# Kernel tuning notes

Hardware: AMD Instinct MI355X
Metric: run time of the kernel (lower is better)

The kernel has to match this reference:

```python
import jax, jax.numpy as jnp
import numpy as np

EMBED_DIM = 1024
NUM_HEADS = 16
HEAD_DIM = EMBED_DIM // NUM_HEADS
MAX_REL = 64
B, S = 4, 1024


def setup_inputs() -> dict:
    key = jax.random.key(0)
    ks = jax.random.split(key, 12)
    scale = 1.0 / np.sqrt(EMBED_DIM)
    inp = {
        "query": jax.random.normal(ks[0], (B, S, EMBED_DIM), jnp.float32),
        "key": jax.random.normal(ks[1], (B, S, EMBED_DIM), jnp.float32),
        "value": jax.random.normal(ks[2], (B, S, EMBED_DIM), jnp.float32),
        "attn_mask": jnp.ones((B, 1, S, S), jnp.int32),
        # projection weights stored [in, out] so x @ W matches torch Linear(x) with W = weight.T
        "Wq": jax.random.normal(ks[3], (EMBED_DIM, EMBED_DIM), jnp.float32) * scale,
        "bq": jnp.zeros((EMBED_DIM,), jnp.float32),
        "Wk": jax.random.normal(ks[4], (EMBED_DIM, EMBED_DIM), jnp.float32) * scale,
        "bk": jnp.zeros((EMBED_DIM,), jnp.float32),
        "Wv": jax.random.normal(ks[5], (EMBED_DIM, EMBED_DIM), jnp.float32) * scale,
        "bv": jnp.zeros((EMBED_DIM,), jnp.float32),
        "Wo": jax.random.normal(ks[6], (EMBED_DIM, EMBED_DIM), jnp.float32) * scale,
        "bo": jnp.zeros((EMBED_DIM,), jnp.float32),
        "rel_pos_embed": jax.random.normal(ks[7], (2 * MAX_REL + 1, HEAD_DIM), jnp.float32) * 0.02,
    }
    return inp


def _split_heads(x):
    # [B, S, E] -> [B, H, S, D]
    b, s, _ = x.shape
    return x.reshape(b, s, NUM_HEADS, HEAD_DIM).transpose(0, 2, 1, 3)


def reference(query, key, value, attn_mask, Wq, bq, Wk, bk, Wv, bv, Wo, bo, rel_pos_embed):
    q = _split_heads(query @ Wq + bq)
    k = _split_heads(key @ Wk + bk)
    v = _split_heads(value @ Wv + bv)

    scores = jnp.einsum("bhqd,bhkd->bhqk", q, k) / np.sqrt(HEAD_DIM).astype(np.float32)

    # relative position bias: rel_pos[i, j] = rel_pos_embed[clip(i - j) + MAX_REL]
    seq_len = scores.shape[-1]
    rng = jnp.arange(seq_len)
    range_mat = jnp.clip(rng[:, None] - rng[None, :], -MAX_REL, MAX_REL) + MAX_REL
    rel_pos = rel_pos_embed[range_mat]                       # [S, S, D]
    # torch: matmul(q[...,None,:], rel_pos.mT).squeeze(-2) == einsum over head_dim (NOT scaled)
    rel_scores = jnp.einsum("bhid,ijd->bhij", q, rel_pos)
    scores = scores + rel_scores

    scores = jnp.where(attn_mask == 0, -jnp.inf, scores)
    attn_weights = jax.nn.softmax(scores, axis=-1)           # dropout p=0.0 -> identity

    out = jnp.einsum("bhqk,bhkd->bhqd", attn_weights, v)
    out = out.transpose(0, 2, 1, 3).reshape(query.shape[0], -1, EMBED_DIM)
    out = out @ Wo + bo
    return out, attn_weights
```

## Files before the change

### kernel.cpp

```cpp
#include <hip/hip_runtime.h>
#include <math.h>

#define BB 4
#define SS 1024
#define EE 1024
#define HH 16
#define DD 64
#define RR 129
#define PRELW 130

typedef __attribute__((ext_vector_type(4))) float f32x4;
typedef __attribute__((ext_vector_type(8))) short bf8;
typedef __attribute__((ext_vector_type(4))) short s4v;

#define MFMA(a, b, c) __builtin_amdgcn_mfma_f32_16x16x32_bf16(a, b, c, 0, 0, 0)

__device__ __forceinline__ float bf2f(unsigned short u) {
    return __uint_as_float(((unsigned)u) << 16);
}
__device__ __forceinline__ unsigned short f2bf(float x) {
    unsigned u = __float_as_uint(x);
    return (unsigned short)((u + 0x7fffu + ((u >> 16) & 1u)) >> 16);
}

__global__ __launch_bounds__(256, 4)
void wtrans_kernel(const float* __restrict__ Wq, const float* __restrict__ Wk,
                   const float* __restrict__ Wv, const float* __restrict__ Wo,
                   unsigned short* __restrict__ wt_hi, unsigned short* __restrict__ wt_lo)
{
    __shared__ float T[64][65];
    const int w = blockIdx.z;
    const float* W = w == 0 ? Wq : (w == 1 ? Wk : (w == 2 ? Wv : Wo));
    const int n0 = blockIdx.x * 64, k0 = blockIdx.y * 64;
    const int tid = threadIdx.x;
#pragma unroll
    for (int i = 0; i < 4; ++i) {
        int c = tid + 256 * i; int r = c >> 4, c4 = c & 15;
        f32x4 v = *(const f32x4*)(W + (size_t)(k0 + r) * EE + n0 + c4 * 4);
        T[r][c4 * 4 + 0] = v.x; T[r][c4 * 4 + 1] = v.y;
        T[r][c4 * 4 + 2] = v.z; T[r][c4 * 4 + 3] = v.w;
    }
    __syncthreads();
#pragma unroll
    for (int i = 0; i < 4; ++i) {
        int c = tid + 256 * i; int r = c >> 4, c4 = c & 15;
        float x0 = T[c4 * 4 + 0][r], x1 = T[c4 * 4 + 1][r];
        float x2 = T[c4 * 4 + 2][r], x3 = T[c4 * 4 + 3][r];
        unsigned short h0 = f2bf(x0), h1 = f2bf(x1), h2 = f2bf(x2), h3 = f2bf(x3);
        unsigned short l0 = f2bf(x0 - bf2f(h0)), l1 = f2bf(x1 - bf2f(h1));
        unsigned short l2 = f2bf(x2 - bf2f(h2)), l3 = f2bf(x3 - bf2f(h3));
        size_t o = (size_t)w * 1048576 + (size_t)(n0 + r) * 1024 + k0 + c4 * 4;
        *(s4v*)&wt_hi[o] = (s4v){(short)h0, (short)h1, (short)h2, (short)h3};
        *(s4v*)&wt_lo[o] = (s4v){(short)l0, (short)l1, (short)l2, (short)l3};
    }
}

__global__ __launch_bounds__(256)
void maskbits_kernel(const int* __restrict__ mask, unsigned long long* __restrict__ mb)
{
    const int w = blockIdx.x * 256 + threadIdx.x;
    const int* p = mask + (size_t)w * 64;
    unsigned long long bits = 0;
#pragma unroll
    for (int i = 0; i < 16; ++i) {
        int4 v = *(const int4*)(p + i * 4);
        bits |= (unsigned long long)(v.x != 0) << (i * 4 + 0);
        bits |= (unsigned long long)(v.y != 0) << (i * 4 + 1);
        bits |= (unsigned long long)(v.z != 0) << (i * 4 + 2);
        bits |= (unsigned long long)(v.w != 0) << (i * 4 + 3);
    }
    mb[w] = bits;
}

template<int ASRC, int EPI>
__device__ __forceinline__ void gemm_body(
    const float* __restrict__ Af,
    const unsigned short* __restrict__ Ah_g, const unsigned short* __restrict__ Al_g,
    const unsigned short* __restrict__ Bh_g, const unsigned short* __restrict__ Bl_g,
    const float* __restrict__ bias,
    float* __restrict__ Yf, unsigned short* __restrict__ Yh, unsigned short* __restrict__ Yl,
    unsigned short* As_h, unsigned short* As_l, unsigned short* Bs_h, unsigned short* Bs_l,
    int m0, int n0)
{
    const int tid = threadIdx.x, lane = tid & 63, wid = tid >> 6;
    const int wm = (wid >> 1) * 64, wn = (wid & 1) * 64;
    f32x4 zero4 = {0.f, 0.f, 0.f, 0.f};
    f32x4 acc[4][4];
#pragma unroll
    for (int a = 0; a < 4; ++a)
#pragma unroll
        for (int b = 0; b < 4; ++b) acc[a][b] = zero4;

    for (int kt = 0; kt < 1024; kt += 64) {
        __syncthreads();
        if (ASRC == 0) {
#pragma unroll
            for (int i = 0; i < 8; ++i) {
                int c = tid + 256 * i; int r = c >> 4, c4 = c & 15;
                f32x4 v = *(const f32x4*)(Af + (size_t)(m0 + r) * 1024 + kt + c4 * 4);
                unsigned short h0 = f2bf(v.x), h1 = f2bf(v.y), h2 = f2bf(v.z), h3 = f2bf(v.w);
                unsigned short l0 = f2bf(v.x - bf2f(h0)), l1 = f2bf(v.y - bf2f(h1));
                unsigned short l2 = f2bf(v.z - bf2f(h2)), l3 = f2bf(v.w - bf2f(h3));
                int off = r * 64 + (((c4 >> 1) ^ (r & 7)) * 8) + (c4 & 1) * 4;
                *(s4v*)&As_h[off] = (s4v){(short)h0, (short)h1, (short)h2, (short)h3};
                *(s4v*)&As_l[off] = (s4v){(short)l0, (short)l1, (short)l2, (short)l3};
            }
        } else {
#pragma unroll
            for (int i = 0; i < 4; ++i) {
                int c = tid + 256 * i; int r = c >> 3, cc = c & 7;
                int off = r * 64 + ((cc ^ (r & 7)) * 8);
                *(bf8*)&As_h[off] = *(const bf8*)(Ah_g + (size_t)(m0 + r) * 1024 + kt + cc * 8);
                *(bf8*)&As_l[off] = *(const bf8*)(Al_g + (size_t)(m0 + r) * 1024 + kt + cc * 8);
            }
        }
#pragma unroll
        for (int i = 0; i < 4; ++i) {
            int c = tid + 256 * i; int r = c >> 3, cc = c & 7;
            int off = r * 64 + ((cc ^ (r & 7)) * 8);
            *(bf8*)&Bs_h[off] = *(const bf8*)(Bh_g + (size_t)(n0 + r) * 1024 + kt + cc * 8);
            *(bf8*)&Bs_l[off] = *(const bf8*)(Bl_g + (size_t)(n0 + r) * 1024 + kt + cc * 8);
        }
        __syncthreads();
#pragma unroll
        for (int ks = 0; ks < 2; ++ks) {
            bf8 ah[4], al[4], bh[4], bl[4];
#pragma unroll
            for (int f = 0; f < 4; ++f) {
                int ra = wm + f * 16 + (lane & 15);
                int ca = (ks * 4 + (lane >> 4)) ^ (ra & 7);
                ah[f] = *(const bf8*)&As_h[ra * 64 + ca * 8];
                al[f] = *(const bf8*)&As_l[ra * 64 + ca * 8];
                int rb = wn + f * 16 + (lane & 15);
                int cb = (ks * 4 + (lane >> 4)) ^ (rb & 7);
                bh[f] = *(const bf8*)&Bs_h[rb * 64 + cb * 8];
                bl[f] = *(const bf8*)&Bs_l[rb * 64 + cb * 8];
            }
#pragma unroll
            for (int fi = 0; fi < 4; ++fi)
#pragma unroll
                for (int fj = 0; fj < 4; ++fj) {
                    acc[fi][fj] = MFMA(ah[fi], bh[fj], acc[fi][fj]);
                    acc[fi][fj] = MFMA(al[fi], bh[fj], acc[fi][fj]);
                    acc[fi][fj] = MFMA(ah[fi], bl[fj], acc[fi][fj]);
                }
        }
    }
#pragma unroll
    for (int fi = 0; fi < 4; ++fi)
#pragma unroll
        for (int fj = 0; fj < 4; ++fj)
#pragma unroll
            for (int rg = 0; rg < 4; ++rg) {
                int m = m0 + wm + fi * 16 + ((lane >> 4) << 2) + rg;
                int n = n0 + wn + fj * 16 + (lane & 15);
                float val = acc[fi][fj][rg] + bias[n];
                if (EPI == 0) {
                    int b = m >> 10, s = m & 1023, h = n >> 6, d = n & 63;
                    size_t o = (((size_t)(b * 16 + h)) * 1024 + s) * 64 + d;
                    unsigned short hv = f2bf(val);
                    unsigned short lv = f2bf(val - bf2f(hv));
                    Yh[o] = hv; Yl[o] = lv;
                } else {
                    Yf[(size_t)m * 1024 + n] = val;
                }
            }
}

__global__ __launch_bounds__(256, 2)
void proj_qkv_kernel(const float* __restrict__ q_in, const float* __restrict__ k_in,
                     const float* __restrict__ v_in,
                     const unsigned short* __restrict__ wt_hi, const unsigned short* __restrict__ wt_lo,
                     const float* __restrict__ bq, const float* __restrict__ bk,
                     const float* __restrict__ bv,
                     unsigned short* qh_hi, unsigned short* qh_lo,
                     unsigned short* kh_hi, unsigned short* kh_lo,
                     unsigned short* vh_hi, unsigned short* vh_lo)
{
    __shared__ __align__(16) unsigned short As_h[128 * 64], As_l[128 * 64];
    __shared__ __align__(16) unsigned short Bs_h[128 * 64], Bs_l[128 * 64];
    const int z = blockIdx.z;
    const float* X = z == 0 ? q_in : (z == 1 ? k_in : v_in);
    const float* bias = z == 0 ? bq : (z == 1 ? bk : bv);
    unsigned short* Yh = z == 0 ? qh_hi : (z == 1 ? kh_hi : vh_hi);
    unsigned short* Yl = z == 0 ? qh_lo : (z == 1 ? kh_lo : vh_lo);
    gemm_body<0, 0>(X, nullptr, nullptr,
                    wt_hi + (size_t)z * 1048576, wt_lo + (size_t)z * 1048576,
                    bias, nullptr, Yh, Yl, As_h, As_l, Bs_h, Bs_l,
                    blockIdx.x * 128, blockIdx.y * 128);
}

__global__ __launch_bounds__(256, 2)
void outproj_kernel(const unsigned short* __restrict__ ctx_hi, const unsigned short* __restrict__ ctx_lo,
                    const unsigned short* __restrict__ wo_hi, const unsigned short* __restrict__ wo_lo,
                    const float* __restrict__ bo, float* __restrict__ out)
{
    __shared__ __align__(16) unsigned short As_h[128 * 64], As_l[128 * 64];
    __shared__ __align__(16) unsigned short Bs_h[128 * 64], Bs_l[128 * 64];
    gemm_body<1, 1>(nullptr, ctx_hi, ctx_lo, wo_hi, wo_lo, bo, out, nullptr, nullptr,
                    As_h, As_l, Bs_h, Bs_l, blockIdx.x * 128, blockIdx.y * 128);
}

__global__ __launch_bounds__(256, 4)
void vtrans_kernel(const unsigned short* __restrict__ vh_hi, const unsigned short* __restrict__ vh_lo,
                   unsigned short* __restrict__ vt_hi, unsigned short* __restrict__ vt_lo)
{
    __shared__ unsigned short T[64][72];
    const unsigned short* src = blockIdx.z ? vh_lo : vh_hi;
    unsigned short* dst = blockIdx.z ? vt_lo : vt_hi;
    const int st = blockIdx.x * 64, bh = blockIdx.y, tid = threadIdx.x;
#pragma unroll
    for (int i = 0; i < 4; ++i) {
        int c = tid + 256 * i; int r = c >> 4, d4 = c & 15;
        s4v v = *(const s4v*)(src + ((size_t)bh * 1024 + st + r) * 64 + d4 * 4);
        T[r][d4 * 4 + 0] = (unsigned short)v.x; T[r][d4 * 4 + 1] = (unsigned short)v.y;
        T[r][d4 * 4 + 2] = (unsigned short)v.z; T[r][d4 * 4 + 3] = (unsigned short)v.w;
    }
    __syncthreads();
#pragma unroll
    for (int i = 0; i < 4; ++i) {
        int c = tid + 256 * i; int r = c >> 4, s4_ = c & 15;
        s4v o = {(short)T[s4_ * 4 + 0][r], (short)T[s4_ * 4 + 1][r],
                 (short)T[s4_ * 4 + 2][r], (short)T[s4_ * 4 + 3][r]};
        *(s4v*)(dst + ((size_t)bh * 64 + r) * 1024 + st + s4_ * 4) = o;
    }
}

__global__ __launch_bounds__(256, 2)
void relproj_kernel(const unsigned short* __restrict__ qh_hi, const float* __restrict__ emb,
                    unsigned short* __restrict__ prel)
{
    __shared__ float se[RR][68];
    __shared__ float sq[128][68];
    const int tid = threadIdx.x;
    const size_t row0 = (size_t)blockIdx.x * 128;
    for (int i = tid; i < RR * 64; i += 256) { int r = i >> 6, d = i & 63; se[r][d] = emb[i]; }
#pragma unroll
    for (int i = 0; i < 8; ++i) {
        int c = tid + 256 * i; int r = c >> 4, d4 = c & 15;
        s4v v = *(const s4v*)(qh_hi + (row0 + r) * 64 + d4 * 4);
        sq[r][d4 * 4 + 0] = bf2f((unsigned short)v.x);
        sq[r][d4 * 4 + 1] = bf2f((unsigned short)v.y);
        sq[r][d4 * 4 + 2] = bf2f((unsigned short)v.z);
        sq[r][d4 * 4 + 3] = bf2f((unsigned short)v.w);
    }
    __syncthreads();
    for (int idx = tid; idx < 128 * RR; idx += 256) {
        int r = idx / RR, c = idx - r * RR;
        const float* a = sq[r];
        const float* b = se[c];
        float s = 0.f;
#pragma unroll
        for (int d = 0; d < 64; ++d) s = fmaf(a[d], b[d], s);
        prel[(row0 + r) * PRELW + c] = f2bf(s);
    }
}

__global__ __launch_bounds__(256, 2)
void scores_kernel(const unsigned short* __restrict__ qh_hi, const unsigned short* __restrict__ qh_lo,
                   const unsigned short* __restrict__ kh_hi, const unsigned short* __restrict__ kh_lo,
                   const unsigned short* __restrict__ prel, const unsigned long long* __restrict__ mb,
                   float* __restrict__ attn, float* __restrict__ rowm, float* __restrict__ rowsum)
{
    __shared__ __align__(16) unsigned short Sh[128 * 64], Sl[128 * 64];
    __shared__ __align__(16) unsigned short Pr[128 * PRELW];
    __shared__ float Sm[2][128], Ss[2][128];
    const int tid = threadIdx.x, lane = tid & 63, wid = tid >> 6;
    const int wi = wid >> 1, wj = wid & 1;
    const int g = lane >> 4, li = lane & 15;
    const int i0 = blockIdx.x * 128, bh = blockIdx.y, b = bh >> 4;

    const unsigned short* qbh = qh_hi + ((size_t)bh * 1024 + i0) * 64;
    const unsigned short* qbl = qh_lo + ((size_t)bh * 1024 + i0) * 64;
#pragma unroll
    for (int i = 0; i < 4; ++i) {
        int c = tid + 256 * i; int r = c >> 3, cc = c & 7;
        int off = r * 64 + ((cc ^ (r & 7)) * 8);
        *(bf8*)&Sh[off] = *(const bf8*)(qbh + r * 64 + cc * 8);
        *(bf8*)&Sl[off] = *(const bf8*)(qbl + r * 64 + cc * 8);
    }
    {
        const unsigned* src = (const unsigned*)(prel + ((size_t)bh * 1024 + i0) * PRELW);
        unsigned* dst = (unsigned*)Pr;
        for (int idx = tid; idx < 128 * (PRELW / 2); idx += 256) dst[idx] = src[idx];
    }
    __syncthreads();
    bf8 qfh[4][2], qfl[4][2];
#pragma unroll
    for (int fi = 0; fi < 4; ++fi)
#pragma unroll
        for (int ks = 0; ks < 2; ++ks) {
            int rb = wi * 64 + fi * 16 + li;
            int cb = (ks * 4 + g) ^ (rb & 7);
            qfh[fi][ks] = *(const bf8*)&Sh[rb * 64 + cb * 8];
            qfl[fi][ks] = *(const bf8*)&Sl[rb * 64 + cb * 8];
        }

    float rm[4], rs[4];
#pragma unroll
    for (int i = 0; i < 4; ++i) { rm[i] = -3.0e38f; rs[i] = 0.f; }

    for (int jt = 0; jt < 8; ++jt) {
        __syncthreads();
        const unsigned short* kbh = kh_hi + ((size_t)bh * 1024 + jt * 128) * 64;
        const unsigned short* kbl = kh_lo + ((size_t)bh * 1024 + jt * 128) * 64;
#pragma unroll
        for (int i = 0; i < 4; ++i) {
            int c = tid + 256 * i; int r = c >> 3, cc = c & 7;
            int off = r * 64 + ((cc ^ (r & 7)) * 8);
            *(bf8*)&Sh[off] = *(const bf8*)(kbh + r * 64 + cc * 8);
            *(bf8*)&Sl[off] = *(const bf8*)(kbl + r * 64 + cc * 8);
        }
        __syncthreads();
        f32x4 zero4 = {0.f, 0.f, 0.f, 0.f};
        f32x4 acc[4][4];
#pragma unroll
        for (int a = 0; a < 4; ++a)
#pragma unroll
            for (int c = 0; c < 4; ++c) acc[a][c] = zero4;
#pragma unroll
        for (int ks = 0; ks < 2; ++ks) {
            bf8 kfh[4], kfl[4];
#pragma unroll
            for (int fj = 0; fj < 4; ++fj) {
                int ra = wj * 64 + fj * 16 + li;
                int ca = (ks * 4 + g) ^ (ra & 7);
                kfh[fj] = *(const bf8*)&Sh[ra * 64 + ca * 8];
                kfl[fj] = *(const bf8*)&Sl[ra * 64 + ca * 8];
            }
#pragma unroll
            for (int fj = 0; fj < 4; ++fj)
#pragma unroll
                for (int fi = 0; fi < 4; ++fi) {
                    acc[fj][fi] = MFMA(kfh[fj], qfh[fi][ks], acc[fj][fi]);
                    acc[fj][fi] = MFMA(kfl[fj], qfh[fi][ks], acc[fj][fi]);
                    acc[fj][fi] = MFMA(kfh[fj], qfl[fi][ks], acc[fj][fi]);
                }
        }
#pragma unroll
        for (int fi = 0; fi < 4; ++fi) {
            const int rowL = wi * 64 + fi * 16 + li;
            const int ii = i0 + rowL;
            const unsigned long long mw = mb[((size_t)b * 1024 + ii) * 16 + jt * 2 + wj];
            float p16[4][4];
            float tmax = -3.0e38f;
#pragma unroll
            for (int fj = 0; fj < 4; ++fj)
#pragma unroll
                for (int rg = 0; rg < 4; ++rg) {
                    int jloc = fj * 16 + g * 4 + rg;
                    int jj = jt * 128 + wj * 64 + jloc;
                    int dd = ii - jj; dd = dd < -64 ? -64 : (dd > 64 ? 64 : dd);
                    float s = acc[fj][fi][rg] * 0.125f + bf2f(Pr[rowL * PRELW + dd + 64]);
                    if (!((mw >> jloc) & 1ull)) s = -1.0e30f;
                    p16[fj][rg] = s;
                    tmax = fmaxf(tmax, s);
                }
            tmax = fmaxf(tmax, __shfl_xor(tmax, 16, 64));
            tmax = fmaxf(tmax, __shfl_xor(tmax, 32, 64));
            float nm = fmaxf(rm[fi], tmax);
            float ps = 0.f;
#pragma unroll
            for (int fj = 0; fj < 4; ++fj)
#pragma unroll
                for (int rg = 0; rg < 4; ++rg) ps += __expf(p16[fj][rg] - nm);
            ps += __shfl_xor(ps, 16, 64);
            ps += __shfl_xor(ps, 32, 64);
            rs[fi] = rs[fi] * __expf(rm[fi] - nm) + ps;
            rm[fi] = nm;
            float* arow = attn + ((size_t)bh * 1024 + ii) * 1024 + jt * 128 + wj * 64 + g * 4;
#pragma unroll
            for (int fj = 0; fj < 4; ++fj) {
                f32x4 st = {p16[fj][0], p16[fj][1], p16[fj][2], p16[fj][3]};
                *(f32x4*)(arow + fj * 16) = st;
            }
        }
    }
#pragma unroll
    for (int fi = 0; fi < 4; ++fi) {
        if (lane < 16) {
            Sm[wj][wi * 64 + fi * 16 + li] = rm[fi];
            Ss[wj][wi * 64 + fi * 16 + li] = rs[fi];
        }
    }
    __syncthreads();
    if (tid < 128) {
        float m0_ = Sm[0][tid], m1_ = Sm[1][tid];
        float mm = fmaxf(m0_, m1_);
        float ss = Ss[0][tid] * __expf(m0_ - mm) + Ss[1][tid] * __expf(m1_ - mm);
        rowm[(size_t)bh * 1024 + i0 + tid] = mm;
        rowsum[(size_t)bh * 1024 + i0 + tid] = ss;
    }
}

__global__ __launch_bounds__(256, 2)
void pv_kernel(float* __restrict__ attn,
               const unsigned short* __restrict__ vt_hi, const unsigned short* __restrict__ vt_lo,
               const float* __restrict__ rowm, const float* __restrict__ rowsum,
               unsigned short* __restrict__ ctx_hi, unsigned short* __restrict__ ctx_lo)
{
    __shared__ __align__(16) unsigned short Ah[128 * 64], Al[128 * 64];
    __shared__ __align__(16) unsigned short Bh_[64 * 64], Bl_[64 * 64];
    const int tid = threadIdx.x, lane = tid & 63, wid = tid >> 6;
    const int i0 = blockIdx.x * 128, bh = blockIdx.y;

    float m8[8], inv8[8];
#pragma unroll
    for (int i = 0; i < 8; ++i) {
        int r = (tid >> 4) + 16 * i;
        m8[i] = rowm[(size_t)bh * 1024 + i0 + r];
        inv8[i] = 1.f / rowsum[(size_t)bh * 1024 + i0 + r];
    }
    f32x4 zero4 = {0.f, 0.f, 0.f, 0.f};
    f32x4 acc[2][4];
#pragma unroll
    for (int a = 0; a < 2; ++a)
#pragma unroll
        for (int c = 0; c < 4; ++c) acc[a][c] = zero4;

    for (int jt = 0; jt < 16; ++jt) {
        __syncthreads();
#pragma unroll
        for (int i = 0; i < 8; ++i) {
            int c = tid + 256 * i; int r = c >> 4, c4 = c & 15;
            size_t gidx = ((size_t)bh * 1024 + i0 + r) * 1024 + jt * 64 + c4 * 4;
            f32x4 v = *(f32x4*)(attn + gidx);
            float mm = m8[i], iv = inv8[i];
            v.x = __expf(v.x - mm) * iv; v.y = __expf(v.y - mm) * iv;
            v.z = __expf(v.z - mm) * iv; v.w = __expf(v.w - mm) * iv;
            *(f32x4*)(attn + gidx) = v;
            unsigned short h0 = f2bf(v.x), h1 = f2bf(v.y), h2 = f2bf(v.z), h3 = f2bf(v.w);
            unsigned short l0 = f2bf(v.x - bf2f(h0)), l1 = f2bf(v.y - bf2f(h1));
            unsigned short l2 = f2bf(v.z - bf2f(h2)), l3 = f2bf(v.w - bf2f(h3));
            int off = r * 64 + (((c4 >> 1) ^ (r & 7)) * 8) + (c4 & 1) * 4;
            *(s4v*)&Ah[off] = (s4v){(short)h0, (short)h1, (short)h2, (short)h3};
            *(s4v*)&Al[off] = (s4v){(short)l0, (short)l1, (short)l2, (short)l3};
        }
#pragma unroll
        for (int i = 0; i < 2; ++i) {
            int c = tid + 256 * i; int r = c >> 3, cc = c & 7;
            int off = r * 64 + ((cc ^ (r & 7)) * 8);
            *(bf8*)&Bh_[off] = *(const bf8*)(vt_hi + ((size_t)bh * 64 + r) * 1024 + jt * 64 + cc * 8);
            *(bf8*)&Bl_[off] = *(const bf8*)(vt_lo + ((size_t)bh * 64 + r) * 1024 + jt * 64 + cc * 8);
        }
        __syncthreads();
#pragma unroll
        for (int ks = 0; ks < 2; ++ks) {
            bf8 ah[2], al[2], bhf[4], blf[4];
#pragma unroll
            for (int f = 0; f < 2; ++f) {
                int ra = wid * 32 + f * 16 + (lane & 15);
                int ca = (ks * 4 + (lane >> 4)) ^ (ra & 7);
                ah[f] = *(const bf8*)&Ah[ra * 64 + ca * 8];
                al[f] = *(const bf8*)&Al[ra * 64 + ca * 8];
            }
#pragma unroll
            for (int f = 0; f < 4; ++f) {
                int rb = f * 16 + (lane & 15);
                int cb = (ks * 4 + (lane >> 4)) ^ (rb & 7);
                bhf[f] = *(const bf8*)&Bh_[rb * 64 + cb * 8];
                blf[f] = *(const bf8*)&Bl_[rb * 64 + cb * 8];
            }
#pragma unroll
            for (int fi = 0; fi < 2; ++fi)
#pragma unroll
                for (int fj = 0; fj < 4; ++fj) {
                    acc[fi][fj] = MFMA(ah[fi], bhf[fj], acc[fi][fj]);
                    acc[fi][fj] = MFMA(al[fi], bhf[fj], acc[fi][fj]);
                    acc[fi][fj] = MFMA(ah[fi], blf[fj], acc[fi][fj]);
                }
        }
    }
    const int b = bh >> 4, h = bh & 15;
#pragma unroll
    for (int fi = 0; fi < 2; ++fi)
#pragma unroll
        for (int fj = 0; fj < 4; ++fj)
#pragma unroll
            for (int rg = 0; rg < 4; ++rg) {
                int ii = i0 + wid * 32 + fi * 16 + ((lane >> 4) << 2) + rg;
                int d = fj * 16 + (lane & 15);
                float val = acc[fi][fj][rg];
                size_t o = ((size_t)b * 1024 + ii) * 1024 + h * 64 + d;
                unsigned short hv = f2bf(val);
                unsigned short lv = f2bf(val - bf2f(hv));
                ctx_hi[o] = hv; ctx_lo[o] = lv;
            }
}

extern "C" void kernel_launch(void* const* d_in, const int* in_sizes, int n_in,
                              void* d_out, int out_size, void* d_ws, size_t ws_size,
                              hipStream_t stream)
{
    const float* query = (const float*)d_in[0];
    const float* key_  = (const float*)d_in[1];
    const float* value = (const float*)d_in[2];
    const int*   mask  = (const int*)d_in[3];
    const float* Wq = (const float*)d_in[4];
    const float* bq = (const float*)d_in[5];
    const float* Wk = (const float*)d_in[6];
    const float* bk = (const float*)d_in[7];
    const float* Wv = (const float*)d_in[8];
    const float* bv = (const float*)d_in[9];
    const float* Wo = (const float*)d_in[10];
    const float* bo = (const float*)d_in[11];
    const float* emb = (const float*)d_in[12];

    unsigned short* wt_hi = (unsigned short*)d_ws;
    unsigned short* wt_lo = wt_hi + (size_t)4 * 1048576;
    unsigned short* qh_hi = wt_lo + (size_t)4 * 1048576;
    unsigned short* qh_lo = qh_hi + 4194304;
    unsigned short* kh_hi = qh_lo + 4194304;
    unsigned short* kh_lo = kh_hi + 4194304;
    unsigned short* vt_hi = kh_lo + 4194304;
    unsigned short* vt_lo = vt_hi + 4194304;
    unsigned short* prel  = vt_lo + 4194304;
    float* rowm   = (float*)d_ws;
    float* rowsum = rowm + 65536;
    unsigned long long* mb = (unsigned long long*)(rowsum + 65536);
    unsigned short* ctx_hi = qh_hi;
    unsigned short* ctx_lo = qh_lo;
    unsigned short* vh_hi = (unsigned short*)d_out;
    unsigned short* vh_lo = vh_hi + 4194304;

    float* out  = (float*)d_out;
    float* attn = (float*)d_out + 4194304;

    dim3 blk(256);
    wtrans_kernel<<<dim3(16, 16, 4), blk, 0, stream>>>(Wq, Wk, Wv, Wo, wt_hi, wt_lo);
    proj_qkv_kernel<<<dim3(32, 8, 3), blk, 0, stream>>>(query, key_, value, wt_hi, wt_lo,
                                                        bq, bk, bv, qh_hi, qh_lo,
                                                        kh_hi, kh_lo, vh_hi, vh_lo);
    maskbits_kernel<<<dim3(256), blk, 0, stream>>>(mask, mb);
    vtrans_kernel<<<dim3(16, 64, 2), blk, 0, stream>>>(vh_hi, vh_lo, vt_hi, vt_lo);
    relproj_kernel<<<dim3(512), blk, 0, stream>>>(qh_hi, emb, prel);
    scores_kernel<<<dim3(8, 64), blk, 0, stream>>>(qh_hi, qh_lo, kh_hi, kh_lo, prel, mb,
                                                   attn, rowm, rowsum);
    pv_kernel<<<dim3(8, 64), blk, 0, stream>>>(attn, vt_hi, vt_lo, rowm, rowsum, ctx_hi, ctx_lo);
    outproj_kernel<<<dim3(32, 8), blk, 0, stream>>>(ctx_hi, ctx_lo,
                                                    wt_hi + (size_t)3 * 1048576,
                                                    wt_lo + (size_t)3 * 1048576, bo, out);
}
```

Baseline: 487.6 us.

## Load PV MFMA operands directly from global memory, dropping LDS staging and barriers

The PV kernel stops staging softmax probabilities and V tiles through shared memory. Each lane now reads its own 8 attention scores per MFMA fragment straight from global memory, normalizes them, writes them back, and packs them into bf16 hi/lo operands in registers, and V fragments are loaded directly from global memory. This removes LDS traffic and the two __syncthreads per tile. In exchange, V fragments are re-read by every wave instead of being shared across the block, and the per-lane global access pattern is less coalesced.

```diff
diff --git a/kernel.cpp b/kernel.cpp
--- a/kernel.cpp
+++ b/kernel.cpp
@@ -399,18 +399,22 @@
                const float* __restrict__ rowm, const float* __restrict__ rowsum,
                unsigned short* __restrict__ ctx_hi, unsigned short* __restrict__ ctx_lo)
 {
-    __shared__ __align__(16) unsigned short Ah[128 * 64], Al[128 * 64];
-    __shared__ __align__(16) unsigned short Bh_[64 * 64], Bl_[64 * 64];
     const int tid = threadIdx.x, lane = tid & 63, wid = tid >> 6;
+    const int g = lane >> 4, li = lane & 15;
     const int i0 = blockIdx.x * 128, bh = blockIdx.y;
 
-    float m8[8], inv8[8];
-#pragma unroll
-    for (int i = 0; i < 8; ++i) {
-        int r = (tid >> 4) + 16 * i;
-        m8[i] = rowm[(size_t)bh * 1024 + i0 + r];
-        inv8[i] = 1.f / rowsum[(size_t)bh * 1024 + i0 + r];
-    }
+    float mmv[2], ivv[2];
+    float* arow[2];
+#pragma unroll
+    for (int fi = 0; fi < 2; ++fi) {
+        const int rr = wid * 32 + fi * 16 + li;
+        mmv[fi] = rowm[(size_t)bh * 1024 + i0 + rr];
+        ivv[fi] = 1.f / rowsum[(size_t)bh * 1024 + i0 + rr];
+        arow[fi] = attn + ((size_t)bh * 1024 + i0 + rr) * 1024 + g * 8;
+    }
+    const unsigned short* vbh = vt_hi + (size_t)bh * 65536 + (size_t)li * 1024 + g * 8;
+    const unsigned short* vbl = vt_lo + (size_t)bh * 65536 + (size_t)li * 1024 + g * 8;
+
     f32x4 zero4 = {0.f, 0.f, 0.f, 0.f};
     f32x4 acc[2][4];
 #pragma unroll
@@ -418,57 +422,40 @@
 #pragma unroll
         for (int c = 0; c < 4; ++c) acc[a][c] = zero4;
 
-    for (int jt = 0; jt < 16; ++jt) {
-        __syncthreads();
-#pragma unroll
-        for (int i = 0; i < 8; ++i) {
-            int c = tid + 256 * i; int r = c >> 4, c4 = c & 15;
-            size_t gidx = ((size_t)bh * 1024 + i0 + r) * 1024 + jt * 64 + c4 * 4;
-            f32x4 v = *(f32x4*)(attn + gidx);
-            float mm = m8[i], iv = inv8[i];
-            v.x = __expf(v.x - mm) * iv; v.y = __expf(v.y - mm) * iv;
-            v.z = __expf(v.z - mm) * iv; v.w = __expf(v.w - mm) * iv;
-            *(f32x4*)(attn + gidx) = v;
-            unsigned short h0 = f2bf(v.x), h1 = f2bf(v.y), h2 = f2bf(v.z), h3 = f2bf(v.w);
-            unsigned short l0 = f2bf(v.x - bf2f(h0)), l1 = f2bf(v.y - bf2f(h1));
-            unsigned short l2 = f2bf(v.z - bf2f(h2)), l3 = f2bf(v.w - bf2f(h3));
-            int off = r * 64 + (((c4 >> 1) ^ (r & 7)) * 8) + (c4 & 1) * 4;
-            *(s4v*)&Ah[off] = (s4v){(short)h0, (short)h1, (short)h2, (short)h3};
-            *(s4v*)&Al[off] = (s4v){(short)l0, (short)l1, (short)l2, (short)l3};
-        }
-#pragma unroll
-        for (int i = 0; i < 2; ++i) {
-            int c = tid + 256 * i; int r = c >> 3, cc = c & 7;
-            int off = r * 64 + ((cc ^ (r & 7)) * 8);
-            *(bf8*)&Bh_[off] = *(const bf8*)(vt_hi + ((size_t)bh * 64 + r) * 1024 + jt * 64 + cc * 8);
-            *(bf8*)&Bl_[off] = *(const bf8*)(vt_lo + ((size_t)bh * 64 + r) * 1024 + jt * 64 + cc * 8);
-        }
-        __syncthreads();
-#pragma unroll
-        for (int ks = 0; ks < 2; ++ks) {
-            bf8 ah[2], al[2], bhf[4], blf[4];
-#pragma unroll
-            for (int f = 0; f < 2; ++f) {
-                int ra = wid * 32 + f * 16 + (lane & 15);
-                int ca = (ks * 4 + (lane >> 4)) ^ (ra & 7);
-                ah[f] = *(const bf8*)&Ah[ra * 64 + ca * 8];
-                al[f] = *(const bf8*)&Al[ra * 64 + ca * 8];
-            }
-#pragma unroll
-            for (int f = 0; f < 4; ++f) {
-                int rb = f * 16 + (lane & 15);
-                int cb = (ks * 4 + (lane >> 4)) ^ (rb & 7);
-                bhf[f] = *(const bf8*)&Bh_[rb * 64 + cb * 8];
-                blf[f] = *(const bf8*)&Bl_[rb * 64 + cb * 8];
-            }
-#pragma unroll
-            for (int fi = 0; fi < 2; ++fi)
-#pragma unroll
-                for (int fj = 0; fj < 4; ++fj) {
-                    acc[fi][fj] = MFMA(ah[fi], bhf[fj], acc[fi][fj]);
-                    acc[fi][fj] = MFMA(al[fi], bhf[fj], acc[fi][fj]);
-                    acc[fi][fj] = MFMA(ah[fi], blf[fj], acc[fi][fj]);
-                }
+    for (int jc = 0; jc < 32; ++jc) {
+        bf8 ah[2], al[2];
+#pragma unroll
+        for (int fi = 0; fi < 2; ++fi) {
+            float* ap = arow[fi] + jc * 32;
+            f32x4 v0 = *(const f32x4*)ap;
+            f32x4 v1 = *(const f32x4*)(ap + 4);
+            const float mm = mmv[fi], iv = ivv[fi];
+            float p0 = __expf(v0.x - mm) * iv, p1 = __expf(v0.y - mm) * iv;
+            float p2 = __expf(v0.z - mm) * iv, p3 = __expf(v0.w - mm) * iv;
+            float p4 = __expf(v1.x - mm) * iv, p5 = __expf(v1.y - mm) * iv;
+            float p6 = __expf(v1.z - mm) * iv, p7 = __expf(v1.w - mm) * iv;
+            f32x4 o0 = {p0, p1, p2, p3}, o1 = {p4, p5, p6, p7};
+            *(f32x4*)ap = o0;
+            *(f32x4*)(ap + 4) = o1;
+            unsigned short h0 = f2bf(p0), h1 = f2bf(p1), h2 = f2bf(p2), h3 = f2bf(p3);
+            unsigned short h4 = f2bf(p4), h5 = f2bf(p5), h6 = f2bf(p6), h7 = f2bf(p7);
+            ah[fi] = (bf8){(short)h0, (short)h1, (short)h2, (short)h3,
+                           (short)h4, (short)h5, (short)h6, (short)h7};
+            al[fi] = (bf8){(short)f2bf(p0 - bf2f(h0)), (short)f2bf(p1 - bf2f(h1)),
+                           (short)f2bf(p2 - bf2f(h2)), (short)f2bf(p3 - bf2f(h3)),
+                           (short)f2bf(p4 - bf2f(h4)), (short)f2bf(p5 - bf2f(h5)),
+                           (short)f2bf(p6 - bf2f(h6)), (short)f2bf(p7 - bf2f(h7))};
+        }
+#pragma unroll
+        for (int fj = 0; fj < 4; ++fj) {
+            bf8 bh_ = *(const bf8*)(vbh + (size_t)fj * 16384 + jc * 32);
+            bf8 bl_ = *(const bf8*)(vbl + (size_t)fj * 16384 + jc * 32);
+#pragma unroll
+            for (int fi = 0; fi < 2; ++fi) {
+                acc[fi][fj] = MFMA(ah[fi], bh_, acc[fi][fj]);
+                acc[fi][fj] = MFMA(al[fi], bh_, acc[fi][fj]);
+                acc[fi][fj] = MFMA(ah[fi], bl_, acc[fi][fj]);
+            }
         }
     }
     const int b = bh >> 4, h = bh & 15;
@@ -478,8 +465,8 @@
         for (int fj = 0; fj < 4; ++fj)
 #pragma unroll
             for (int rg = 0; rg < 4; ++rg) {
-                int ii = i0 + wid * 32 + fi * 16 + ((lane >> 4) << 2) + rg;
-                int d = fj * 16 + (lane & 15);
+                int ii = i0 + wid * 32 + fi * 16 + g * 4 + rg;
+                int d = fj * 16 + li;
                 float val = acc[fi][fj][rg];
                 size_t o = ((size_t)b * 1024 + ii) * 1024 + h * 64 + d;
                 unsigned short hv = f2bf(val);
```

After: 547.2 us. 12.2% more time.

## Fuse relpos projection, scores, softmax and PV into one two-pass attention kernel

Applied to the files above, without the earlier changes.

Merges relproj, scores and pv into a single kernel. The relative-position projection now runs on MFMA inside the block. A first pass over K computes row max and sum. A second pass recomputes QK^T, writes the normalized attention once, and feeds the probabilities through lane shuffles straight into the PV MFMAs. This removes the write-then-read-modify-write of the 64 MB attention matrix and the prel and rowm/rowsum round trips. In exchange the QK^T work is done twice, V is read from global memory without LDS staging, and register pressure rises.

```diff
diff --git a/kernel.cpp b/kernel.cpp
--- a/kernel.cpp
+++ b/kernel.cpp
@@ -10,6 +10,7 @@
 #define PRELW 130
 
 typedef __attribute__((ext_vector_type(4))) float f32x4;
+typedef __attribute__((ext_vector_type(4))) int   i32x4;
 typedef __attribute__((ext_vector_type(8))) short bf8;
 typedef __attribute__((ext_vector_type(4))) short s4v;
 
@@ -227,48 +228,21 @@
 }
 
 __global__ __launch_bounds__(256, 2)
-void relproj_kernel(const unsigned short* __restrict__ qh_hi, const float* __restrict__ emb,
-                    unsigned short* __restrict__ prel)
-{
-    __shared__ float se[RR][68];
-    __shared__ float sq[128][68];
-    const int tid = threadIdx.x;
-    const size_t row0 = (size_t)blockIdx.x * 128;
-    for (int i = tid; i < RR * 64; i += 256) { int r = i >> 6, d = i & 63; se[r][d] = emb[i]; }
-#pragma unroll
-    for (int i = 0; i < 8; ++i) {
-        int c = tid + 256 * i; int r = c >> 4, d4 = c & 15;
-        s4v v = *(const s4v*)(qh_hi + (row0 + r) * 64 + d4 * 4);
-        sq[r][d4 * 4 + 0] = bf2f((unsigned short)v.x);
-        sq[r][d4 * 4 + 1] = bf2f((unsigned short)v.y);
-        sq[r][d4 * 4 + 2] = bf2f((unsigned short)v.z);
-        sq[r][d4 * 4 + 3] = bf2f((unsigned short)v.w);
-    }
-    __syncthreads();
-    for (int idx = tid; idx < 128 * RR; idx += 256) {
-        int r = idx / RR, c = idx - r * RR;
-        const float* a = sq[r];
-        const float* b = se[c];
-        float s = 0.f;
-#pragma unroll
-        for (int d = 0; d < 64; ++d) s = fmaf(a[d], b[d], s);
-        prel[(row0 + r) * PRELW + c] = f2bf(s);
-    }
-}
-
-__global__ __launch_bounds__(256, 2)
-void scores_kernel(const unsigned short* __restrict__ qh_hi, const unsigned short* __restrict__ qh_lo,
-                   const unsigned short* __restrict__ kh_hi, const unsigned short* __restrict__ kh_lo,
-                   const unsigned short* __restrict__ prel, const unsigned long long* __restrict__ mb,
-                   float* __restrict__ attn, float* __restrict__ rowm, float* __restrict__ rowsum)
+void attn_fused_kernel(const unsigned short* __restrict__ qh_hi, const unsigned short* __restrict__ qh_lo,
+                       const unsigned short* __restrict__ kh_hi, const unsigned short* __restrict__ kh_lo,
+                       const unsigned short* __restrict__ vt_hi, const unsigned short* __restrict__ vt_lo,
+                       const float* __restrict__ emb, const unsigned long long* __restrict__ mb,
+                       float* __restrict__ attn,
+                       unsigned short* __restrict__ ctx_hi, unsigned short* __restrict__ ctx_lo)
 {
     __shared__ __align__(16) unsigned short Sh[128 * 64], Sl[128 * 64];
     __shared__ __align__(16) unsigned short Pr[128 * PRELW];
-    __shared__ float Sm[2][128], Ss[2][128];
+    __shared__ float Sm[2][128], Ss[2][128], SmF[128], SsF[128];
     const int tid = threadIdx.x, lane = tid & 63, wid = tid >> 6;
     const int wi = wid >> 1, wj = wid & 1;
     const int g = lane >> 4, li = lane & 15;
     const int i0 = blockIdx.x * 128, bh = blockIdx.y, b = bh >> 4;
+    const f32x4 zero4 = {0.f, 0.f, 0.f, 0.f};
 
     const unsigned short* qbh = qh_hi + ((size_t)bh * 1024 + i0) * 64;
     const unsigned short* qbl = qh_lo + ((size_t)bh * 1024 + i0) * 64;
@@ -279,12 +253,8 @@
         *(bf8*)&Sh[off] = *(const bf8*)(qbh + r * 64 + cc * 8);
         *(bf8*)&Sl[off] = *(const bf8*)(qbl + r * 64 + cc * 8);
     }
-    {
-        const unsigned* src = (const unsigned*)(prel + ((size_t)bh * 1024 + i0) * PRELW);
-        unsigned* dst = (unsigned*)Pr;
-        for (int idx = tid; idx < 128 * (PRELW / 2); idx += 256) dst[idx] = src[idx];
-    }
-    __syncthreads();
+    __syncthreads();
+
     bf8 qfh[4][2], qfl[4][2];
 #pragma unroll
     for (int fi = 0; fi < 4; ++fi)
@@ -296,6 +266,30 @@
             qfl[fi][ks] = *(const bf8*)&Sl[rb * 64 + cb * 8];
         }
 
+    for (int t = wid; t < 72; t += 4) {
+        const int it = t / 9, rt = t % 9;
+        f32x4 pc = zero4;
+#pragma unroll
+        for (int ks = 0; ks < 2; ++ks) {
+            int ra = it * 16 + li;
+            int ca = (ks * 4 + g) ^ (ra & 7);
+            bf8 aq = *(const bf8*)&Sh[ra * 64 + ca * 8];
+            int er = rt * 16 + li; if (er > 128) er = 128;
+            const float* ep = emb + (size_t)er * 64 + ks * 32 + g * 8;
+            f32x4 e0 = *(const f32x4*)ep;
+            f32x4 e1 = *(const f32x4*)(ep + 4);
+            bf8 be = {(short)f2bf(e0.x), (short)f2bf(e0.y), (short)f2bf(e0.z), (short)f2bf(e0.w),
+                      (short)f2bf(e1.x), (short)f2bf(e1.y), (short)f2bf(e1.z), (short)f2bf(e1.w)};
+            pc = MFMA(aq, be, pc);
+        }
+        const int rcol = rt * 16 + li;
+        if (rcol < RR) {
+#pragma unroll
+            for (int rg = 0; rg < 4; ++rg)
+                Pr[(it * 16 + g * 4 + rg) * PRELW + rcol] = f2bf(pc[rg]);
+        }
+    }
+
     float rm[4], rs[4];
 #pragma unroll
     for (int i = 0; i < 4; ++i) { rm[i] = -3.0e38f; rs[i] = 0.f; }
@@ -312,7 +306,6 @@
             *(bf8*)&Sl[off] = *(const bf8*)(kbl + r * 64 + cc * 8);
         }
         __syncthreads();
-        f32x4 zero4 = {0.f, 0.f, 0.f, 0.f};
         f32x4 acc[4][4];
 #pragma unroll
         for (int a = 0; a < 4; ++a)
@@ -368,12 +361,6 @@
             ps += __shfl_xor(ps, 32, 64);
             rs[fi] = rs[fi] * __expf(rm[fi] - nm) + ps;
             rm[fi] = nm;
-            float* arow = attn + ((size_t)bh * 1024 + ii) * 1024 + jt * 128 + wj * 64 + g * 4;
-#pragma unroll
-            for (int fj = 0; fj < 4; ++fj) {
-                f32x4 st = {p16[fj][0], p16[fj][1], p16[fj][2], p16[fj][3]};
-                *(f32x4*)(arow + fj * 16) = st;
-            }
         }
     }
 #pragma unroll
@@ -386,106 +373,157 @@
     __syncthreads();
     if (tid < 128) {
         float m0_ = Sm[0][tid], m1_ = Sm[1][tid];
-        float mm = fmaxf(m0_, m1_);
-        float ss = Ss[0][tid] * __expf(m0_ - mm) + Ss[1][tid] * __expf(m1_ - mm);
-        rowm[(size_t)bh * 1024 + i0 + tid] = mm;
-        rowsum[(size_t)bh * 1024 + i0 + tid] = ss;
-    }
-}
-
-__global__ __launch_bounds__(256, 2)
-void pv_kernel(float* __restrict__ attn,
-               const unsigned short* __restrict__ vt_hi, const unsigned short* __restrict__ vt_lo,
-               const float* __restrict__ rowm, const float* __restrict__ rowsum,
-               unsigned short* __restrict__ ctx_hi, unsigned short* __restrict__ ctx_lo)
-{
-    __shared__ __align__(16) unsigned short Ah[128 * 64], Al[128 * 64];
-    __shared__ __align__(16) unsigned short Bh_[64 * 64], Bl_[64 * 64];
-    const int tid = threadIdx.x, lane = tid & 63, wid = tid >> 6;
-    const int i0 = blockIdx.x * 128, bh = blockIdx.y;
-
-    float m8[8], inv8[8];
-#pragma unroll
-    for (int i = 0; i < 8; ++i) {
-        int r = (tid >> 4) + 16 * i;
-        m8[i] = rowm[(size_t)bh * 1024 + i0 + r];
-        inv8[i] = 1.f / rowsum[(size_t)bh * 1024 + i0 + r];
-    }
-    f32x4 zero4 = {0.f, 0.f, 0.f, 0.f};
-    f32x4 acc[2][4];
-#pragma unroll
-    for (int a = 0; a < 2; ++a)
-#pragma unroll
-        for (int c = 0; c < 4; ++c) acc[a][c] = zero4;
-
-    for (int jt = 0; jt < 16; ++jt) {
+        float mmx = fmaxf(m0_, m1_);
+        SmF[tid] = mmx;
+        SsF[tid] = Ss[0][tid] * __expf(m0_ - mmx) + Ss[1][tid] * __expf(m1_ - mmx);
+    }
+    __syncthreads();
+    float mm4[4], iv4[4];
+#pragma unroll
+    for (int fi = 0; fi < 4; ++fi) {
+        mm4[fi] = SmF[wi * 64 + fi * 16 + li];
+        iv4[fi] = 1.f / SsF[wi * 64 + fi * 16 + li];
+    }
+
+    f32x4 ctx_acc[4][4];
+#pragma unroll
+    for (int a = 0; a < 4; ++a)
+#pragma unroll
+        for (int c = 0; c < 4; ++c) ctx_acc[a][c] = zero4;
+
+    for (int jt = 0; jt < 8; ++jt) {
         __syncthreads();
-#pragma unroll
-        for (int i = 0; i < 8; ++i) {
-            int c = tid + 256 * i; int r = c >> 4, c4 = c & 15;
-            size_t gidx = ((size_t)bh * 1024 + i0 + r) * 1024 + jt * 64 + c4 * 4;
-            f32x4 v = *(f32x4*)(attn + gidx);
-            float mm = m8[i], iv = inv8[i];
-            v.x = __expf(v.x - mm) * iv; v.y = __expf(v.y - mm) * iv;
-            v.z = __expf(v.z - mm) * iv; v.w = __expf(v.w - mm) * iv;
-            *(f32x4*)(attn + gidx) = v;
-            unsigned short h0 = f2bf(v.x), h1 = f2bf(v.y), h2 = f2bf(v.z), h3 = f2bf(v.w);
-            unsigned short l0 = f2bf(v.x - bf2f(h0)), l1 = f2bf(v.y - bf2f(h1));
-            unsigned short l2 = f2bf(v.z - bf2f(h2)), l3 = f2bf(v.w - bf2f(h3));
-            int off = r * 64 + (((c4 >> 1) ^ (r & 7)) * 8) + (c4 & 1) * 4;
-            *(s4v*)&Ah[off] = (s4v){(short)h0, (short)h1, (short)h2, (short)h3};
-            *(s4v*)&Al[off] = (s4v){(short)l0, (short)l1, (short)l2, (short)l3};
-        }
-#pragma unroll
-        for (int i = 0; i < 2; ++i) {
+        const unsigned short* kbh = kh_hi + ((size_t)bh * 1024 + jt * 128) * 64;
+        const unsigned short* kbl = kh_lo + ((size_t)bh * 1024 + jt * 128) * 64;
+#pragma unroll
+        for (int i = 0; i < 4; ++i) {
             int c = tid + 256 * i; int r = c >> 3, cc = c & 7;
             int off = r * 64 + ((cc ^ (r & 7)) * 8);
-            *(bf8*)&Bh_[off] = *(const bf8*)(vt_hi + ((size_t)bh * 64 + r) * 1024 + jt * 64 + cc * 8);
-            *(bf8*)&Bl_[off] = *(const bf8*)(vt_lo + ((size_t)bh * 64 + r) * 1024 + jt * 64 + cc * 8);
+            *(bf8*)&Sh[off] = *(const bf8*)(kbh + r * 64 + cc * 8);
+            *(bf8*)&Sl[off] = *(const bf8*)(kbl + r * 64 + cc * 8);
         }
         __syncthreads();
+        f32x4 acc[4][4];
+#pragma unroll
+        for (int a = 0; a < 4; ++a)
+#pragma unroll
+            for (int c = 0; c < 4; ++c) acc[a][c] = zero4;
 #pragma unroll
         for (int ks = 0; ks < 2; ++ks) {
-            bf8 ah[2], al[2], bhf[4], blf[4];
-#pragma unroll
-            for (int f = 0; f < 2; ++f) {
-                int ra = wid * 32 + f * 16 + (lane & 15);
-                int ca = (ks * 4 + (lane >> 4)) ^ (ra & 7);
-                ah[f] = *(const bf8*)&Ah[ra * 64 + ca * 8];
-                al[f] = *(const bf8*)&Al[ra * 64 + ca * 8];
-            }
-#pragma unroll
-            for (int f = 0; f < 4; ++f) {
-                int rb = f * 16 + (lane & 15);
-                int cb = (ks * 4 + (lane >> 4)) ^ (rb & 7);
-                bhf[f] = *(const bf8*)&Bh_[rb * 64 + cb * 8];
-                blf[f] = *(const bf8*)&Bl_[rb * 64 + cb * 8];
-            }
-#pragma unroll
-            for (int fi = 0; fi < 2; ++fi)
-#pragma unroll
-                for (int fj = 0; fj < 4; ++fj) {
-                    acc[fi][fj] = MFMA(ah[fi], bhf[fj], acc[fi][fj]);
-                    acc[fi][fj] = MFMA(al[fi], bhf[fj], acc[fi][fj]);
-                    acc[fi][fj] = MFMA(ah[fi], blf[fj], acc[fi][fj]);
-                }
-        }
-    }
-    const int b = bh >> 4, h = bh & 15;
-#pragma unroll
-    for (int fi = 0; fi < 2; ++fi)
-#pragma unroll
-        for (int fj = 0; fj < 4; ++fj)
-#pragma unroll
-            for (int rg = 0; rg < 4; ++rg) {
-                int ii = i0 + wid * 32 + fi * 16 + ((lane >> 4) << 2) + rg;
-                int d = fj * 16 + (lane & 15);
-                float val = acc[fi][fj][rg];
-                size_t o = ((size_t)b * 1024 + ii) * 1024 + h * 64 + d;
-                unsigned short hv = f2bf(val);
-                unsigned short lv = f2bf(val - bf2f(hv));
-                ctx_hi[o] = hv; ctx_lo[o] = lv;
-            }
+            bf8 kfh[4], kfl[4];
+#pragma unroll
+            for (int fj = 0; fj < 4; ++fj) {
+                int ra = wj * 64 + fj * 16 + li;
+                int ca = (ks * 4 + g) ^ (ra & 7);
+                kfh[fj] = *(const bf8*)&Sh[ra * 64 + ca * 8];
+                kfl[fj] = *(const bf8*)&Sl[ra * 64 + ca * 8];
+            }
+#pragma unroll
+            for (int fj = 0; fj < 4; ++fj)
+#pragma unroll
+                for (int fi = 0; fi < 4; ++fi) {
+                    acc[fj][fi] = MFMA(kfh[fj], qfh[fi][ks], acc[fj][fi]);
+                    acc[fj][fi] = MFMA(kfl[fj], qfh[fi][ks], acc[fj][fi]);
+                    acc[fj][fi] = MFMA(kfh[fj], qfl[fi][ks], acc[fj][fi]);
+                }
+        }
+#pragma unroll
+        for (int c = 0; c < 2; ++c) {
+            bf8 vfh[4], vfl[4];
+#pragma unroll
+            for (int fd = 0; fd < 4; ++fd) {
+                size_t vb = (size_t)bh * 65536 + (size_t)(fd * 16 + li) * 1024
+                          + jt * 128 + wj * 64 + c * 32 + g * 8;
+                vfh[fd] = *(const bf8*)(vt_hi + vb);
+                vfl[fd] = *(const bf8*)(vt_lo + vb);
+            }
+#pragma unroll
+            for (int fi = 0; fi < 4; ++fi) {
+                const int rowL = wi * 64 + fi * 16 + li;
+                const int ii = i0 + rowL;
+                const unsigned long long mw = mb[((size_t)b * 1024 + ii) * 16 + jt * 2 + wj];
+                const float mmf = mm4[fi], ivf = iv4[fi];
+                float* arow = attn + ((size_t)bh * 1024 + ii) * 1024 + jt * 128 + wj * 64 + g * 4;
+                unsigned wh[2][2], wl[2][2];
+#pragma unroll
+                for (int t = 0; t < 2; ++t) {
+                    const int fj = c * 2 + t;
+                    f32x4 pv;
+#pragma unroll
+                    for (int rg = 0; rg < 4; ++rg) {
+                        int jloc = fj * 16 + g * 4 + rg;
+                        int jj = jt * 128 + wj * 64 + jloc;
+                        int dd = ii - jj; dd = dd < -64 ? -64 : (dd > 64 ? 64 : dd);
+                        float s = acc[fj][fi][rg] * 0.125f + bf2f(Pr[rowL * PRELW + dd + 64]);
+                        if (!((mw >> jloc) & 1ull)) s = -1.0e30f;
+                        pv[rg] = __expf(s - mmf) * ivf;
+                    }
+                    *(f32x4*)(arow + fj * 16) = pv;
+                    unsigned short h0 = f2bf(pv.x), h1 = f2bf(pv.y), h2 = f2bf(pv.z), h3 = f2bf(pv.w);
+                    wh[t][0] = (unsigned)h0 | ((unsigned)h1 << 16);
+                    wh[t][1] = (unsigned)h2 | ((unsigned)h3 << 16);
+                    unsigned short l0 = f2bf(pv.x - bf2f(h0)), l1 = f2bf(pv.y - bf2f(h1));
+                    unsigned short l2 = f2bf(pv.z - bf2f(h2)), l3 = f2bf(pv.w - bf2f(h3));
+                    wl[t][0] = (unsigned)l0 | ((unsigned)l1 << 16);
+                    wl[t][1] = (unsigned)l2 | ((unsigned)l3 << 16);
+                }
+                const int src0 = ((g & 1) * 2) * 16 + li;
+                const int src1 = src0 + 16;
+                const bool hiT = (g >> 1) & 1;
+                int x0A = __shfl((int)wh[0][0], src0, 64), x0B = __shfl((int)wh[1][0], src0, 64);
+                int x1A = __shfl((int)wh[0][1], src0, 64), x1B = __shfl((int)wh[1][1], src0, 64);
+                int x2A = __shfl((int)wh[0][0], src1, 64), x2B = __shfl((int)wh[1][0], src1, 64);
+                int x3A = __shfl((int)wh[0][1], src1, 64), x3B = __shfl((int)wh[1][1], src1, 64);
+                i32x4 awh = {hiT ? x0B : x0A, hiT ? x1B : x1A, hiT ? x2B : x2A, hiT ? x3B : x3A};
+                bf8 pah = *(bf8*)&awh;
+                int y0A = __shfl((int)wl[0][0], src0, 64), y0B = __shfl((int)wl[1][0], src0, 64);
+                int y1A = __shfl((int)wl[0][1], src0, 64), y1B = __shfl((int)wl[1][1], src0, 64);
+                int y2A = __shfl((int)wl[0][0], src1, 64), y2B = __shfl((int)wl[1][0], src1, 64);
+                int y3A = __shfl((int)wl[0][1], src1, 64), y3B = __shfl((int)wl[1][1], src1, 64);
+                i32x4 awl = {hiT ? y0B : y0A, hiT ? y1B : y1A, hiT ? y2B : y2A, hiT ? y3B : y3A};
+                bf8 pal = *(bf8*)&awl;
+#pragma unroll
+                for (int fd = 0; fd < 4; ++fd) {
+                    ctx_acc[fi][fd] = MFMA(pah, vfh[fd], ctx_acc[fi][fd]);
+                    ctx_acc[fi][fd] = MFMA(pal, vfh[fd], ctx_acc[fi][fd]);
+                    ctx_acc[fi][fd] = MFMA(pah, vfl[fd], ctx_acc[fi][fd]);
+                }
+            }
+        }
+    }
+
+    __syncthreads();
+    float* red = (wi == 0) ? (float*)Sh : (float*)Sl;
+    if (wj == 1) {
+#pragma unroll
+        for (int fi = 0; fi < 4; ++fi)
+#pragma unroll
+            for (int fd = 0; fd < 4; ++fd)
+#pragma unroll
+                for (int rg = 0; rg < 4; ++rg) {
+                    int idx = (fi * 4 + fd) * 4 + rg;
+                    red[lane * 64 + ((idx + lane) & 63)] = ctx_acc[fi][fd][rg];
+                }
+    }
+    __syncthreads();
+    if (wj == 0) {
+        const int b_ = bh >> 4, h = bh & 15;
+#pragma unroll
+        for (int fi = 0; fi < 4; ++fi)
+#pragma unroll
+            for (int fd = 0; fd < 4; ++fd)
+#pragma unroll
+                for (int rg = 0; rg < 4; ++rg) {
+                    int idx = (fi * 4 + fd) * 4 + rg;
+                    float val = ctx_acc[fi][fd][rg] + red[lane * 64 + ((idx + lane) & 63)];
+                    int ii = i0 + wi * 64 + fi * 16 + g * 4 + rg;
+                    int d = fd * 16 + li;
+                    size_t o = ((size_t)b_ * 1024 + ii) * 1024 + h * 64 + d;
+                    unsigned short hv = f2bf(val);
+                    unsigned short lv = f2bf(val - bf2f(hv));
+                    ctx_hi[o] = hv; ctx_lo[o] = lv;
+                }
+    }
 }
 
 extern "C" void kernel_launch(void* const* d_in, const int* in_sizes, int n_in,
@@ -514,12 +552,9 @@
     unsigned short* kh_lo = kh_hi + 4194304;
     unsigned short* vt_hi = kh_lo + 4194304;
     unsigned short* vt_lo = vt_hi + 4194304;
-    unsigned short* prel  = vt_lo + 4194304;
-    float* rowm   = (float*)d_ws;
-    float* rowsum = rowm + 65536;
-    unsigned long long* mb = (unsigned long long*)(rowsum + 65536);
-    unsigned short* ctx_hi = qh_hi;
-    unsigned short* ctx_lo = qh_lo;
+    unsigned short* ctx_hi = vt_lo + 4194304;
+    unsigned short* ctx_lo = ctx_hi + 4194304;
+    unsigned long long* mb = (unsigned long long*)d_ws;
     unsigned short* vh_hi = (unsigned short*)d_out;
     unsigned short* vh_lo = vh_hi + 4194304;
 
@@ -533,10 +568,9 @@
                                                         kh_hi, kh_lo, vh_hi, vh_lo);
     maskbits_kernel<<<dim3(256), blk, 0, stream>>>(mask, mb);
     vtrans_kernel<<<dim3(16, 64, 2), blk, 0, stream>>>(vh_hi, vh_lo, vt_hi, vt_lo);
-    relproj_kernel<<<dim3(512), blk, 0, stream>>>(qh_hi, emb, prel);
-    scores_kernel<<<dim3(8, 64), blk, 0, stream>>>(qh_hi, qh_lo, kh_hi, kh_lo, prel, mb,
-                                                   attn, rowm, rowsum);
-    pv_kernel<<<dim3(8, 64), blk, 0, stream>>>(attn, vt_hi, vt_lo, rowm, rowsum, ctx_hi, ctx_lo);
+    attn_fused_kernel<<<dim3(8, 64), blk, 0, stream>>>(qh_hi, qh_lo, kh_hi, kh_lo,
+                                                       vt_hi, vt_lo, emb, mb,
+                                                       attn, ctx_hi, ctx_lo);
     outproj_kernel<<<dim3(32, 8), blk, 0, stream>>>(ctx_hi, ctx_lo,
                                                     wt_hi + (size_t)3 * 1048576,
                                                     wt_lo + (size_t)3 * 1048576, bo, out);
```

Result: slower. 538.5 us (+10.4%).
